# Performance work log

Hardware: AMD Instinct MI355X
Metric: run time of the kernel (lower is better)

Reference implementation:

```python
import jax, jax.numpy as jnp
import numpy as np

B, C, H, W = 8, 256, 128, 128
HEADS, DIM_HEAD = 4, 32
HID = HEADS * DIM_HEAD  # 128


def setup_inputs() -> dict:
    key = jax.random.key(0)
    k1, k2, k3, k4 = jax.random.split(key, 4)
    x = jax.random.normal(k1, (B, C, H, W), dtype=jnp.float32)
    # 1x1 conv weights stored as [out_ch, in_ch]
    w_qkv = jax.random.normal(k2, (3 * HID, C), dtype=jnp.float32) * (1.0 / np.sqrt(C))
    w_out = jax.random.normal(k3, (C, HID), dtype=jnp.float32) * (1.0 / np.sqrt(HID))
    b_out = jax.random.normal(k4, (C,), dtype=jnp.float32) * 0.01
    return {"x": x, "w_qkv": w_qkv, "w_out": w_out, "b_out": b_out}


def reference(x, w_qkv, w_out, b_out):
    b, c, h, w = x.shape
    n = h * w
    # 1x1 conv == channel matmul
    qkv = jnp.einsum('oc,bchw->bohw', w_qkv, x)  # [b, 3*HID, h, w]
    q, k, v = jnp.split(qkv, 3, axis=1)
    # rearrange 'b (heads d) h w -> b heads d (h w)'
    def to_heads(t):
        return t.reshape(b, HEADS, DIM_HEAD, n)
    q, k, v = to_heads(q), to_heads(k), to_heads(v)
    k = jax.nn.softmax(k, axis=-1)  # over spatial n
    # q_scale is False: q used as-is
    context = jnp.einsum('bhdn,bhen->bhde', k, v)   # [b, heads, d, e] small
    out = jnp.einsum('bhde,bhdn->bhen', context, q)  # [b, heads, e, n]
    out = out.reshape(b, HID, h, w)
    out = jnp.einsum('oc,bchw->bohw', w_out, out) + b_out[None, :, None, None]
    return out
```

## Files before the change

kernel.cpp:

```cpp
#include <hip/hip_runtime.h>
#include <stdint.h>

#define BB 8
#define CIN 256
#define NSP 16384
#define HID 128

typedef __bf16 bfrag __attribute__((ext_vector_type(8)));
typedef float  f32x4 __attribute__((ext_vector_type(4)));

__device__ __forceinline__ unsigned short f2bf(float f) {
  union { float f; unsigned int u; } v; v.f = f;
  unsigned int u = v.u;
  return (unsigned short)((u + 0x7FFFu + ((u >> 16) & 1u)) >> 16);
}

__global__ __launch_bounds__(256) void la_prep(const float* __restrict__ w_qkv,
                                               unsigned short* __restrict__ wkvb,
                                               float* __restrict__ zbase) {
  const int blk = blockIdx.x;
  const int t = threadIdx.x;
  if (blk < 64) {
    const int off = (blk * 256 + t) * 4;
    const float4 wv4 = *(const float4*)(w_qkv + (size_t)128 * CIN + off);
    ushort4 p;
    p.x = f2bf(wv4.x); p.y = f2bf(wv4.y); p.z = f2bf(wv4.z); p.w = f2bf(wv4.w);
    *(ushort4*)(wkvb + off) = p;
  } else {
    for (int i = t; i < 8448; i += 256) {
      float4 z = {0.f, 0.f, 0.f, 0.f};
      *(float4*)(zbase + i * 4) = z;
    }
  }
}

__global__ __launch_bounds__(512, 4) void la_fused(const float* __restrict__ x,
                                                   const unsigned short* __restrict__ wkvb,
                                                   float* __restrict__ ctxu,
                                                   float* __restrict__ sums) {
  __shared__ __align__(16) union {
    struct { unsigned short Xb[2][128][40]; } g;
    struct { unsigned short Lk[64][136]; unsigned short Lv[64][136];
             float Pc[4][1024]; } e;
  } sh;
  const int chunk = blockIdx.x;
  const int n0 = chunk * 128;
  const int b = blockIdx.y;
  const int t = threadIdx.x;
  const int lane = t & 63, wv = t >> 6;
  const int l15 = lane & 15, q = lane >> 4;
  const int cl = t & 31;
  const int n16 = (t >> 5) * 8;
  const float* xp = x + (size_t)b * CIN * NSP + n0;
  f32x4 acc[2][8];
#pragma unroll
  for (int i = 0; i < 2; ++i)
#pragma unroll
    for (int j = 0; j < 8; ++j) acc[i][j] = 0.0f;

  float4 xa0, xa1;
  {
    const float* xr = xp + (size_t)cl * NSP + n16;
    xa0 = *(const float4*)xr;
    xa1 = *(const float4*)(xr + 4);
  }
  {
    sh.g.Xb[0][n16 + 0][cl] = f2bf(xa0.x);
    sh.g.Xb[0][n16 + 1][cl] = f2bf(xa0.y);
    sh.g.Xb[0][n16 + 2][cl] = f2bf(xa0.z);
    sh.g.Xb[0][n16 + 3][cl] = f2bf(xa0.w);
    sh.g.Xb[0][n16 + 4][cl] = f2bf(xa1.x);
    sh.g.Xb[0][n16 + 5][cl] = f2bf(xa1.y);
    sh.g.Xb[0][n16 + 6][cl] = f2bf(xa1.z);
    sh.g.Xb[0][n16 + 7][cl] = f2bf(xa1.w);
    const float* xr = xp + (size_t)(32 + cl) * NSP + n16;
    xa0 = *(const float4*)xr;
    xa1 = *(const float4*)(xr + 4);
  }
  __syncthreads();

#pragma unroll
  for (int kc = 0; kc < 8; ++kc) {
    const int p = kc & 1;
    bfrag a0 = *(const bfrag*)(wkvb + (size_t)(wv * 16 + l15) * CIN + kc * 32 + q * 8);
    bfrag a1 = *(const bfrag*)(wkvb + (size_t)(128 + wv * 16 + l15) * CIN + kc * 32 + q * 8);
    if (kc < 7) {
      sh.g.Xb[p ^ 1][n16 + 0][cl] = f2bf(xa0.x);
      sh.g.Xb[p ^ 1][n16 + 1][cl] = f2bf(xa0.y);
      sh.g.Xb[p ^ 1][n16 + 2][cl] = f2bf(xa0.z);
      sh.g.Xb[p ^ 1][n16 + 3][cl] = f2bf(xa0.w);
      sh.g.Xb[p ^ 1][n16 + 4][cl] = f2bf(xa1.x);
      sh.g.Xb[p ^ 1][n16 + 5][cl] = f2bf(xa1.y);
      sh.g.Xb[p ^ 1][n16 + 6][cl] = f2bf(xa1.z);
      sh.g.Xb[p ^ 1][n16 + 7][cl] = f2bf(xa1.w);
      if (kc < 6) {
        const float* xr = xp + (size_t)((kc + 2) * 32 + cl) * NSP + n16;
        xa0 = *(const float4*)xr;
        xa1 = *(const float4*)(xr + 4);
      }
    }
#pragma unroll
    for (int ni = 0; ni < 8; ++ni) {
      bfrag bbv = *(const bfrag*)&sh.g.Xb[p][ni * 16 + l15][q * 8];
      acc[0][ni] = __builtin_amdgcn_mfma_f32_16x16x32_bf16(a0, bbv, acc[0][ni], 0, 0, 0);
      acc[1][ni] = __builtin_amdgcn_mfma_f32_16x16x32_bf16(a1, bbv, acc[1][ni], 0, 0, 0);
    }
    __syncthreads();
  }

#pragma unroll
  for (int ni = 0; ni < 8; ++ni)
#pragma unroll
    for (int rg = 0; rg < 4; ++rg) acc[0][ni][rg] = __expf(acc[0][ni][rg]);

  {
    float sp[4] = {0.f, 0.f, 0.f, 0.f};
#pragma unroll
    for (int ni = 0; ni < 8; ++ni)
#pragma unroll
      for (int rg = 0; rg < 4; ++rg) sp[rg] += acc[0][ni][rg];
#pragma unroll
    for (int rg = 0; rg < 4; ++rg) {
      float s = sp[rg];
      s += __shfl_down(s, 8, 16);
      s += __shfl_down(s, 4, 16);
      s += __shfl_down(s, 2, 16);
      s += __shfl_down(s, 1, 16);
      if (l15 == 0) atomicAdd(&sums[b * 128 + wv * 16 + q * 4 + rg], s);
    }
  }
#pragma unroll
  for (int ph = 0; ph < 2; ++ph) {
    if ((wv >> 2) == ph) {
      const int r = (wv & 3) * 16 + q * 4;
#pragma unroll
      for (int ni = 0; ni < 8; ++ni)
#pragma unroll
        for (int rg = 0; rg < 4; ++rg) {
          sh.e.Lk[r + rg][ni * 16 + l15] = f2bf(acc[0][ni][rg]);
          sh.e.Lv[r + rg][ni * 16 + l15] = f2bf(acc[1][ni][rg]);
        }
    }
    __syncthreads();
    const int hl = wv >> 2, nq = wv & 3;
    f32x4 c2[2][2];
    c2[0][0] = 0.f; c2[0][1] = 0.f; c2[1][0] = 0.f; c2[1][1] = 0.f;
    bfrag ka[2], vb[2];
#pragma unroll
    for (int d2 = 0; d2 < 2; ++d2)
      ka[d2] = *(const bfrag*)&sh.e.Lk[hl * 32 + d2 * 16 + l15][nq * 32 + q * 8];
#pragma unroll
    for (int e2 = 0; e2 < 2; ++e2)
      vb[e2] = *(const bfrag*)&sh.e.Lv[hl * 32 + e2 * 16 + l15][nq * 32 + q * 8];
#pragma unroll
    for (int d2 = 0; d2 < 2; ++d2)
#pragma unroll
      for (int e2 = 0; e2 < 2; ++e2)
        c2[d2][e2] = __builtin_amdgcn_mfma_f32_16x16x32_bf16(ka[d2], vb[e2], c2[d2][e2], 0, 0, 0);
    const int slot = hl * 2 + (nq & 1);
    if (nq < 2) {
#pragma unroll
      for (int d2 = 0; d2 < 2; ++d2)
#pragma unroll
        for (int e2 = 0; e2 < 2; ++e2)
#pragma unroll
          for (int rg = 0; rg < 4; ++rg)
            sh.e.Pc[slot][(d2 * 16 + q * 4 + rg) * 32 + e2 * 16 + l15] = c2[d2][e2][rg];
    }
    __syncthreads();
    if (nq >= 2) {
#pragma unroll
      for (int d2 = 0; d2 < 2; ++d2)
#pragma unroll
        for (int e2 = 0; e2 < 2; ++e2)
#pragma unroll
          for (int rg = 0; rg < 4; ++rg)
            sh.e.Pc[slot][(d2 * 16 + q * 4 + rg) * 32 + e2 * 16 + l15] += c2[d2][e2][rg];
    }
    __syncthreads();
    for (int idx = t; idx < 2048; idx += 512) {
      const int h2 = idx >> 10, pos = idx & 1023;
      atomicAdd(&ctxu[(size_t)b * 4096 + (ph * 2 + h2) * 1024 + pos],
                sh.e.Pc[h2 * 2][pos] + sh.e.Pc[h2 * 2 + 1][pos]);
    }
    __syncthreads();
  }
}

__global__ __launch_bounds__(256) void la_mid(const float* __restrict__ w_out,
                                              const float* __restrict__ ctxu,
                                              const float* __restrict__ sums,
                                              const float* __restrict__ w_qkv,
                                              unsigned short* __restrict__ wcomb) {
  __shared__ float wrow[128];
  const int o = blockIdx.x;
  const int b = blockIdx.y;
  const int t = threadIdx.x;
  if (t < 128) {
    const int h = t >> 5, d = t & 31;
    const float* wr = w_out + (size_t)o * HID + h * 32;
    const float* cr = ctxu + ((size_t)(b * 4 + h) * 32 + d) * 32;
    float s = 0.f;
#pragma unroll 8
    for (int e = 0; e < 32; ++e) s += wr[e] * cr[e];
    wrow[t] = s * (1.0f / sums[b * 128 + t]);
  }
  __syncthreads();
  float s = 0.f;
#pragma unroll 8
  for (int hd = 0; hd < 128; ++hd) s += wrow[hd] * w_qkv[(size_t)hd * CIN + t];
  wcomb[((size_t)b * 256 + o) * 256 + t] = f2bf(s);
}

__global__ __launch_bounds__(512, 4) void la_out(const unsigned short* __restrict__ wcomb,
                                                 const float* __restrict__ x,
                                                 const float* __restrict__ b_out,
                                                 float* __restrict__ out) {
  __shared__ __align__(16) unsigned short Bt[2][128][40];
  const int n0 = blockIdx.x * 128;
  const int b = blockIdx.y;
  const int t = threadIdx.x;
  const int lane = t & 63, wv = t >> 6;
  const int l15 = lane & 15, q = lane >> 4;
  const int wm = (wv & 3) * 64;
  const int wn = (wv >> 2) * 64;
  const int cl = t & 31, n16 = (t >> 5) * 8;
  const float* xp = x + (size_t)b * CIN * NSP + n0;
  const unsigned short* abase = wcomb + (size_t)b * 256 * 256;
  f32x4 acc[4][4];
#pragma unroll
  for (int i = 0; i < 4; ++i)
#pragma unroll
    for (int j = 0; j < 4; ++j) acc[i][j] = 0.0f;

  float4 xa0, xa1;
  {
    const float* xr = xp + (size_t)cl * NSP + n16;
    xa0 = *(const float4*)xr;
    xa1 = *(const float4*)(xr + 4);
  }
  {
    Bt[0][n16 + 0][cl] = f2bf(xa0.x);
    Bt[0][n16 + 1][cl] = f2bf(xa0.y);
    Bt[0][n16 + 2][cl] = f2bf(xa0.z);
    Bt[0][n16 + 3][cl] = f2bf(xa0.w);
    Bt[0][n16 + 4][cl] = f2bf(xa1.x);
    Bt[0][n16 + 5][cl] = f2bf(xa1.y);
    Bt[0][n16 + 6][cl] = f2bf(xa1.z);
    Bt[0][n16 + 7][cl] = f2bf(xa1.w);
    const float* xr = xp + (size_t)(32 + cl) * NSP + n16;
    xa0 = *(const float4*)xr;
    xa1 = *(const float4*)(xr + 4);
  }
  __syncthreads();

#pragma unroll
  for (int kc = 0; kc < 8; ++kc) {
    const int p = kc & 1;
    bfrag a[4];
#pragma unroll
    for (int mi = 0; mi < 4; ++mi)
      a[mi] = *(const bfrag*)(abase + (size_t)(wm + mi * 16 + l15) * 256 + kc * 32 + q * 8);
    if (kc < 7) {
      Bt[p ^ 1][n16 + 0][cl] = f2bf(xa0.x);
      Bt[p ^ 1][n16 + 1][cl] = f2bf(xa0.y);
      Bt[p ^ 1][n16 + 2][cl] = f2bf(xa0.z);
      Bt[p ^ 1][n16 + 3][cl] = f2bf(xa0.w);
      Bt[p ^ 1][n16 + 4][cl] = f2bf(xa1.x);
      Bt[p ^ 1][n16 + 5][cl] = f2bf(xa1.y);
      Bt[p ^ 1][n16 + 6][cl] = f2bf(xa1.z);
      Bt[p ^ 1][n16 + 7][cl] = f2bf(xa1.w);
      if (kc < 6) {
        const float* xr = xp + (size_t)((kc + 2) * 32 + cl) * NSP + n16;
        xa0 = *(const float4*)xr;
        xa1 = *(const float4*)(xr + 4);
      }
    }
#pragma unroll
    for (int ni = 0; ni < 4; ++ni) {
      bfrag bbv = *(const bfrag*)&Bt[p][wn + ni * 16 + l15][q * 8];
#pragma unroll
      for (int mi = 0; mi < 4; ++mi)
        acc[mi][ni] = __builtin_amdgcn_mfma_f32_16x16x32_bf16(a[mi], bbv, acc[mi][ni], 0, 0, 0);
    }
    __syncthreads();
  }
  float* obase = out + (size_t)b * 256 * NSP;
#pragma unroll
  for (int mi = 0; mi < 4; ++mi) {
    const int ob = wm + mi * 16 + q * 4;
    const float4 bias = *(const float4*)(b_out + ob);
    float ba[4] = {bias.x, bias.y, bias.z, bias.w};
#pragma unroll
    for (int ni = 0; ni < 4; ++ni) {
      const int n = n0 + wn + ni * 16 + l15;
#pragma unroll
      for (int rg = 0; rg < 4; ++rg)
        obase[(size_t)(ob + rg) * NSP + n] = acc[mi][ni][rg] + ba[rg];
    }
  }
}


extern "C" void kernel_launch(void* const* d_in, const int* in_sizes, int n_in,
                              void* d_out, int out_size, void* d_ws, size_t ws_size,
                              hipStream_t stream) {
  (void)in_sizes; (void)n_in; (void)out_size; (void)ws_size;
  const float* x     = (const float*)d_in[0];
  const float* w_qkv = (const float*)d_in[1];
  const float* w_out = (const float*)d_in[2];
  const float* b_out = (const float*)d_in[3];
  float* out = (float*)d_out;
  char* ws = (char*)d_ws;
  unsigned short* wkvb  = (unsigned short*)(ws);
  float* ctxu           = (float*)(ws + 131072);
  float* sums           = (float*)(ws + 262144);
  unsigned short* wcomb = (unsigned short*)(ws + 266240);

  la_prep<<<dim3(65), dim3(256), 0, stream>>>(w_qkv, wkvb, ctxu);
  la_fused<<<dim3(NSP / 128, BB), dim3(512), 0, stream>>>(x, wkvb, ctxu, sums);
  la_mid<<<dim3(256, BB), dim3(256), 0, stream>>>(w_out, ctxu, sums, w_qkv, wcomb);
  la_out<<<dim3(NSP / 128, BB), dim3(512), 0, stream>>>(wcomb, x, b_out, out);
}
```

Before: 329.3 us.

## Pre-transpose x to bf16 n-major and stream tiles via global_load_lds

Adds a transpose pass that converts x once into a bf16 [b][n][c] workspace, merged with the weight conversion and zeroing kernel. The fused and output GEMM kernels then read this buffer with direct global-to-LDS 16-byte loads into a four-stage XOR-swizzled ring, replacing per-thread fp32 loads, conversion and scattered 2-byte LDS stores. Each GEMM reads half the bytes, but the extra pass writes 64MB and reads the 128MB x once more, which may cost as much as it saves.

```diff
diff --git a/kernel.cpp b/kernel.cpp
--- a/kernel.cpp
+++ b/kernel.cpp
@@ -8,6 +8,7 @@
 
 typedef __bf16 bfrag __attribute__((ext_vector_type(8)));
 typedef float  f32x4 __attribute__((ext_vector_type(4)));
+typedef unsigned short us8 __attribute__((ext_vector_type(8)));
 
 __device__ __forceinline__ unsigned short f2bf(float f) {
   union { float f; unsigned int u; } v; v.f = f;
@@ -15,13 +16,54 @@
   return (unsigned short)((u + 0x7FFFu + ((u >> 16) & 1u)) >> 16);
 }
 
-__global__ __launch_bounds__(256) void la_prep(const float* __restrict__ w_qkv,
-                                               unsigned short* __restrict__ wkvb,
-                                               float* __restrict__ zbase) {
+__device__ __forceinline__ void gload_lds16(const unsigned short* g, unsigned short* l) {
+  __builtin_amdgcn_global_load_lds((const __attribute__((address_space(1))) void*)g,
+                                   (__attribute__((address_space(3))) void*)l, 16, 0, 0);
+}
+
+#define FENCE() asm volatile("" ::: "memory")
+
+__global__ __launch_bounds__(256) void la_xT(const float* __restrict__ x,
+                                             unsigned short* __restrict__ xT,
+                                             const float* __restrict__ w_qkv,
+                                             unsigned short* __restrict__ wkvb,
+                                             float* __restrict__ zbase) {
+  __shared__ float Xs[64][65];
   const int blk = blockIdx.x;
   const int t = threadIdx.x;
-  if (blk < 64) {
-    const int off = (blk * 256 + t) * 4;
+  if (blk < 8192) {
+    const int b = blk >> 10;
+    const int tile = blk & 1023;
+    const int c0 = (tile & 3) * 64;
+    const int n0 = (tile >> 2) * 64;
+    const float* xb = x + (size_t)b * CIN * NSP;
+    {
+      const int c = t >> 2, nf = (t & 3) * 16;
+      const float* xr = xb + (size_t)(c0 + c) * NSP + n0 + nf;
+#pragma unroll
+      for (int i = 0; i < 4; ++i) {
+        const float4 v = *(const float4*)(xr + i * 4);
+        Xs[c][nf + i * 4 + 0] = v.x;
+        Xs[c][nf + i * 4 + 1] = v.y;
+        Xs[c][nf + i * 4 + 2] = v.z;
+        Xs[c][nf + i * 4 + 3] = v.w;
+      }
+    }
+    __syncthreads();
+    {
+      const int n = t >> 2, c16 = (t & 3) * 16;
+      us8 v0, v1;
+#pragma unroll
+      for (int j = 0; j < 8; ++j) {
+        v0[j] = f2bf(Xs[c16 + j][n]);
+        v1[j] = f2bf(Xs[c16 + 8 + j][n]);
+      }
+      unsigned short* orow = xT + ((size_t)b * NSP + n0 + n) * CIN + c0 + c16;
+      *(us8*)orow = v0;
+      *(us8*)(orow + 8) = v1;
+    }
+  } else if (blk < 8256) {
+    const int off = ((blk - 8192) * 256 + t) * 4;
     const float4 wv4 = *(const float4*)(w_qkv + (size_t)128 * CIN + off);
     ushort4 p;
     p.x = f2bf(wv4.x); p.y = f2bf(wv4.y); p.z = f2bf(wv4.z); p.w = f2bf(wv4.w);
@@ -34,12 +76,12 @@
   }
 }
 
-__global__ __launch_bounds__(512, 4) void la_fused(const float* __restrict__ x,
+__global__ __launch_bounds__(512, 4) void la_fused(const unsigned short* __restrict__ xT,
                                                    const unsigned short* __restrict__ wkvb,
                                                    float* __restrict__ ctxu,
                                                    float* __restrict__ sums) {
   __shared__ __align__(16) union {
-    struct { unsigned short Xb[2][128][40]; } g;
+    unsigned short Sx[4][4096];
     struct { unsigned short Lk[64][136]; unsigned short Lv[64][136];
              float Pc[4][1024]; } e;
   } sh;
@@ -49,63 +91,66 @@
   const int t = threadIdx.x;
   const int lane = t & 63, wv = t >> 6;
   const int l15 = lane & 15, q = lane >> 4;
-  const int cl = t & 31;
-  const int n16 = (t >> 5) * 8;
-  const float* xp = x + (size_t)b * CIN * NSP + n0;
+  const int qs = (q ^ ((l15 >> 1) & 3)) * 8;
+  const unsigned short* xTb = xT + ((size_t)b * NSP + n0) * CIN;
+  const int sn = t >> 2, sc8 = t & 3;
+  const int sc8s = sc8 ^ ((sn >> 1) & 3);
+  const unsigned short* sg = xTb + (size_t)sn * CIN + sc8s * 8;
+  unsigned short* sl = &sh.Sx[0][0] + t * 8;
   f32x4 acc[2][8];
 #pragma unroll
   for (int i = 0; i < 2; ++i)
 #pragma unroll
     for (int j = 0; j < 8; ++j) acc[i][j] = 0.0f;
 
-  float4 xa0, xa1;
-  {
-    const float* xr = xp + (size_t)cl * NSP + n16;
-    xa0 = *(const float4*)xr;
-    xa1 = *(const float4*)(xr + 4);
-  }
-  {
-    sh.g.Xb[0][n16 + 0][cl] = f2bf(xa0.x);
-    sh.g.Xb[0][n16 + 1][cl] = f2bf(xa0.y);
-    sh.g.Xb[0][n16 + 2][cl] = f2bf(xa0.z);
-    sh.g.Xb[0][n16 + 3][cl] = f2bf(xa0.w);
-    sh.g.Xb[0][n16 + 4][cl] = f2bf(xa1.x);
-    sh.g.Xb[0][n16 + 5][cl] = f2bf(xa1.y);
-    sh.g.Xb[0][n16 + 6][cl] = f2bf(xa1.z);
-    sh.g.Xb[0][n16 + 7][cl] = f2bf(xa1.w);
-    const float* xr = xp + (size_t)(32 + cl) * NSP + n16;
-    xa0 = *(const float4*)xr;
-    xa1 = *(const float4*)(xr + 4);
-  }
-  __syncthreads();
-
-#pragma unroll
-  for (int kc = 0; kc < 8; ++kc) {
-    const int p = kc & 1;
+  gload_lds16(sg + 0 * 32, sl + 0 * 4096);
+  gload_lds16(sg + 1 * 32, sl + 1 * 4096);
+  asm volatile("s_waitcnt vmcnt(1)" ::: "memory");
+  __builtin_amdgcn_s_barrier();
+  FENCE();
+
+#pragma unroll
+  for (int kc = 0; kc < 6; ++kc) {
     bfrag a0 = *(const bfrag*)(wkvb + (size_t)(wv * 16 + l15) * CIN + kc * 32 + q * 8);
     bfrag a1 = *(const bfrag*)(wkvb + (size_t)(128 + wv * 16 + l15) * CIN + kc * 32 + q * 8);
-    if (kc < 7) {
-      sh.g.Xb[p ^ 1][n16 + 0][cl] = f2bf(xa0.x);
-      sh.g.Xb[p ^ 1][n16 + 1][cl] = f2bf(xa0.y);
-      sh.g.Xb[p ^ 1][n16 + 2][cl] = f2bf(xa0.z);
-      sh.g.Xb[p ^ 1][n16 + 3][cl] = f2bf(xa0.w);
-      sh.g.Xb[p ^ 1][n16 + 4][cl] = f2bf(xa1.x);
-      sh.g.Xb[p ^ 1][n16 + 5][cl] = f2bf(xa1.y);
-      sh.g.Xb[p ^ 1][n16 + 6][cl] = f2bf(xa1.z);
-      sh.g.Xb[p ^ 1][n16 + 7][cl] = f2bf(xa1.w);
-      if (kc < 6) {
-        const float* xr = xp + (size_t)((kc + 2) * 32 + cl) * NSP + n16;
-        xa0 = *(const float4*)xr;
-        xa1 = *(const float4*)(xr + 4);
-      }
-    }
+    gload_lds16(sg + (kc + 2) * 32, sl + ((kc + 2) & 3) * 4096);
+    const unsigned short* bufp = &sh.Sx[kc & 3][0];
 #pragma unroll
     for (int ni = 0; ni < 8; ++ni) {
-      bfrag bbv = *(const bfrag*)&sh.g.Xb[p][ni * 16 + l15][q * 8];
+      bfrag bbv = *(const bfrag*)(bufp + (ni * 16 + l15) * 32 + qs);
       acc[0][ni] = __builtin_amdgcn_mfma_f32_16x16x32_bf16(a0, bbv, acc[0][ni], 0, 0, 0);
       acc[1][ni] = __builtin_amdgcn_mfma_f32_16x16x32_bf16(a1, bbv, acc[1][ni], 0, 0, 0);
     }
-    __syncthreads();
+    asm volatile("s_waitcnt vmcnt(1)" ::: "memory");
+    __builtin_amdgcn_s_barrier();
+    FENCE();
+  }
+  {
+    bfrag a0 = *(const bfrag*)(wkvb + (size_t)(wv * 16 + l15) * CIN + 6 * 32 + q * 8);
+    bfrag a1 = *(const bfrag*)(wkvb + (size_t)(128 + wv * 16 + l15) * CIN + 6 * 32 + q * 8);
+    const unsigned short* bufp = &sh.Sx[2][0];
+#pragma unroll
+    for (int ni = 0; ni < 8; ++ni) {
+      bfrag bbv = *(const bfrag*)(bufp + (ni * 16 + l15) * 32 + qs);
+      acc[0][ni] = __builtin_amdgcn_mfma_f32_16x16x32_bf16(a0, bbv, acc[0][ni], 0, 0, 0);
+      acc[1][ni] = __builtin_amdgcn_mfma_f32_16x16x32_bf16(a1, bbv, acc[1][ni], 0, 0, 0);
+    }
+    asm volatile("s_waitcnt vmcnt(0)" ::: "memory");
+    __builtin_amdgcn_s_barrier();
+    FENCE();
+  }
+  {
+    bfrag a0 = *(const bfrag*)(wkvb + (size_t)(wv * 16 + l15) * CIN + 7 * 32 + q * 8);
+    bfrag a1 = *(const bfrag*)(wkvb + (size_t)(128 + wv * 16 + l15) * CIN + 7 * 32 + q * 8);
+    const unsigned short* bufp = &sh.Sx[3][0];
+#pragma unroll
+    for (int ni = 0; ni < 8; ++ni) {
+      bfrag bbv = *(const bfrag*)(bufp + (ni * 16 + l15) * 32 + qs);
+      acc[0][ni] = __builtin_amdgcn_mfma_f32_16x16x32_bf16(a0, bbv, acc[0][ni], 0, 0, 0);
+      acc[1][ni] = __builtin_amdgcn_mfma_f32_16x16x32_bf16(a1, bbv, acc[1][ni], 0, 0, 0);
+    }
+    __builtin_amdgcn_s_barrier();
+    FENCE();
   }
 
 #pragma unroll
@@ -213,77 +258,85 @@
 }
 
 __global__ __launch_bounds__(512, 4) void la_out(const unsigned short* __restrict__ wcomb,
-                                                 const float* __restrict__ x,
+                                                 const unsigned short* __restrict__ xT,
                                                  const float* __restrict__ b_out,
                                                  float* __restrict__ out) {
-  __shared__ __align__(16) unsigned short Bt[2][128][40];
+  __shared__ __align__(16) unsigned short Sx[4][4096];
   const int n0 = blockIdx.x * 128;
   const int b = blockIdx.y;
   const int t = threadIdx.x;
   const int lane = t & 63, wv = t >> 6;
   const int l15 = lane & 15, q = lane >> 4;
+  const int qs = (q ^ ((l15 >> 1) & 3)) * 8;
   const int wm = (wv & 3) * 64;
   const int wn = (wv >> 2) * 64;
-  const int cl = t & 31, n16 = (t >> 5) * 8;
-  const float* xp = x + (size_t)b * CIN * NSP + n0;
+  const unsigned short* xTb = xT + ((size_t)b * NSP + n0) * CIN;
   const unsigned short* abase = wcomb + (size_t)b * 256 * 256;
+  const int sn = t >> 2, sc8 = t & 3;
+  const int sc8s = sc8 ^ ((sn >> 1) & 3);
+  const unsigned short* sg = xTb + (size_t)sn * CIN + sc8s * 8;
+  unsigned short* sl = &Sx[0][0] + t * 8;
   f32x4 acc[4][4];
 #pragma unroll
   for (int i = 0; i < 4; ++i)
 #pragma unroll
     for (int j = 0; j < 4; ++j) acc[i][j] = 0.0f;
 
-  float4 xa0, xa1;
-  {
-    const float* xr = xp + (size_t)cl * NSP + n16;
-    xa0 = *(const float4*)xr;
-    xa1 = *(const float4*)(xr + 4);
-  }
-  {
-    Bt[0][n16 + 0][cl] = f2bf(xa0.x);
-    Bt[0][n16 + 1][cl] = f2bf(xa0.y);
-    Bt[0][n16 + 2][cl] = f2bf(xa0.z);
-    Bt[0][n16 + 3][cl] = f2bf(xa0.w);
-    Bt[0][n16 + 4][cl] = f2bf(xa1.x);
-    Bt[0][n16 + 5][cl] = f2bf(xa1.y);
-    Bt[0][n16 + 6][cl] = f2bf(xa1.z);
-    Bt[0][n16 + 7][cl] = f2bf(xa1.w);
-    const float* xr = xp + (size_t)(32 + cl) * NSP + n16;
-    xa0 = *(const float4*)xr;
-    xa1 = *(const float4*)(xr + 4);
-  }
-  __syncthreads();
-
-#pragma unroll
-  for (int kc = 0; kc < 8; ++kc) {
-    const int p = kc & 1;
+  gload_lds16(sg + 0 * 32, sl + 0 * 4096);
+  gload_lds16(sg + 1 * 32, sl + 1 * 4096);
+  asm volatile("s_waitcnt vmcnt(1)" ::: "memory");
+  __builtin_amdgcn_s_barrier();
+  FENCE();
+
+#pragma unroll
+  for (int kc = 0; kc < 6; ++kc) {
     bfrag a[4];
 #pragma unroll
     for (int mi = 0; mi < 4; ++mi)
       a[mi] = *(const bfrag*)(abase + (size_t)(wm + mi * 16 + l15) * 256 + kc * 32 + q * 8);
-    if (kc < 7) {
-      Bt[p ^ 1][n16 + 0][cl] = f2bf(xa0.x);
-      Bt[p ^ 1][n16 + 1][cl] = f2bf(xa0.y);
-      Bt[p ^ 1][n16 + 2][cl] = f2bf(xa0.z);
-      Bt[p ^ 1][n16 + 3][cl] = f2bf(xa0.w);
-      Bt[p ^ 1][n16 + 4][cl] = f2bf(xa1.x);
-      Bt[p ^ 1][n16 + 5][cl] = f2bf(xa1.y);
-      Bt[p ^ 1][n16 + 6][cl] = f2bf(xa1.z);
-      Bt[p ^ 1][n16 + 7][cl] = f2bf(xa1.w);
-      if (kc < 6) {
-        const float* xr = xp + (size_t)((kc + 2) * 32 + cl) * NSP + n16;
-        xa0 = *(const float4*)xr;
-        xa1 = *(const float4*)(xr + 4);
-      }
-    }
+    gload_lds16(sg + (kc + 2) * 32, sl + ((kc + 2) & 3) * 4096);
+    const unsigned short* bufp = &Sx[kc & 3][0];
 #pragma unroll
     for (int ni = 0; ni < 4; ++ni) {
-      bfrag bbv = *(const bfrag*)&Bt[p][wn + ni * 16 + l15][q * 8];
+      bfrag bbv = *(const bfrag*)(bufp + (wn + ni * 16 + l15) * 32 + qs);
 #pragma unroll
       for (int mi = 0; mi < 4; ++mi)
         acc[mi][ni] = __builtin_amdgcn_mfma_f32_16x16x32_bf16(a[mi], bbv, acc[mi][ni], 0, 0, 0);
     }
-    __syncthreads();
+    asm volatile("s_waitcnt vmcnt(1)" ::: "memory");
+    __builtin_amdgcn_s_barrier();
+    FENCE();
+  }
+  {
+    bfrag a[4];
+#pragma unroll
+    for (int mi = 0; mi < 4; ++mi)
+      a[mi] = *(const bfrag*)(abase + (size_t)(wm + mi * 16 + l15) * 256 + 6 * 32 + q * 8);
+    const unsigned short* bufp = &Sx[2][0];
+#pragma unroll
+    for (int ni = 0; ni < 4; ++ni) {
+      bfrag bbv = *(const bfrag*)(bufp + (wn + ni * 16 + l15) * 32 + qs);
+#pragma unroll
+      for (int mi = 0; mi < 4; ++mi)
+        acc[mi][ni] = __builtin_amdgcn_mfma_f32_16x16x32_bf16(a[mi], bbv, acc[mi][ni], 0, 0, 0);
+    }
+    asm volatile("s_waitcnt vmcnt(0)" ::: "memory");
+    __builtin_amdgcn_s_barrier();
+    FENCE();
+  }
+  {
+    bfrag a[4];
+#pragma unroll
+    for (int mi = 0; mi < 4; ++mi)
+      a[mi] = *(const bfrag*)(abase + (size_t)(wm + mi * 16 + l15) * 256 + 7 * 32 + q * 8);
+    const unsigned short* bufp = &Sx[3][0];
+#pragma unroll
+    for (int ni = 0; ni < 4; ++ni) {
+      bfrag bbv = *(const bfrag*)(bufp + (wn + ni * 16 + l15) * 32 + qs);
+#pragma unroll
+      for (int mi = 0; mi < 4; ++mi)
+        acc[mi][ni] = __builtin_amdgcn_mfma_f32_16x16x32_bf16(a[mi], bbv, acc[mi][ni], 0, 0, 0);
+    }
   }
   float* obase = out + (size_t)b * 256 * NSP;
 #pragma unroll
@@ -312,13 +365,14 @@
   const float* b_out = (const float*)d_in[3];
   float* out = (float*)d_out;
   char* ws = (char*)d_ws;
-  unsigned short* wkvb  = (unsigned short*)(ws);
-  float* ctxu           = (float*)(ws + 131072);
-  float* sums           = (float*)(ws + 262144);
-  unsigned short* wcomb = (unsigned short*)(ws + 266240);
-
-  la_prep<<<dim3(65), dim3(256), 0, stream>>>(w_qkv, wkvb, ctxu);
-  la_fused<<<dim3(NSP / 128, BB), dim3(512), 0, stream>>>(x, wkvb, ctxu, sums);
+  unsigned short* xTws  = (unsigned short*)(ws);
+  unsigned short* wkvb  = (unsigned short*)(ws + 67108864);
+  float* ctxu           = (float*)(ws + 67239936);
+  float* sums           = (float*)(ws + 67371008);
+  unsigned short* wcomb = (unsigned short*)(ws + 67375104);
+
+  la_xT<<<dim3(8257), dim3(256), 0, stream>>>(x, xTws, w_qkv, wkvb, ctxu);
+  la_fused<<<dim3(NSP / 128, BB), dim3(512), 0, stream>>>(xTws, wkvb, ctxu, sums);
   la_mid<<<dim3(256, BB), dim3(256), 0, stream>>>(w_out, ctxu, sums, w_qkv, wcomb);
-  la_out<<<dim3(NSP / 128, BB), dim3(512), 0, stream>>>(wcomb, x, b_out, out);
-}
+  la_out<<<dim3(NSP / 128, BB), dim3(512), 0, stream>>>(wcomb, xTws, b_out, out);
+}
```

Measured after the change: 353.2 us. 7.3% more time.

## Halve spatial tile to 64 and simplify context reduction in fused kernel

Applied to the files above, without the earlier changes.

Both the fused K/V projection kernel and the output GEMM kernel now process 64 spatial positions per block instead of 128, which doubles the grid and raises the launch-bounds occupancy hint from 4 to 6 blocks per CU. In the fused kernel, each wave now computes a 16x16 context tile directly from shared K/V and atomically adds it to global memory. This drops the two-phase shared-memory partial-sum staging and its extra barriers. The cost is twice as many global atomics on the context buffer and twice as many reloads of weight fragments per unit of spatial work.

```diff
diff --git a/kernel.cpp b/kernel.cpp
--- a/kernel.cpp
+++ b/kernel.cpp
@@ -34,156 +34,101 @@
   }
 }
 
-__global__ __launch_bounds__(512, 4) void la_fused(const float* __restrict__ x,
+__global__ __launch_bounds__(512, 6) void la_fused(const float* __restrict__ x,
                                                    const unsigned short* __restrict__ wkvb,
                                                    float* __restrict__ ctxu,
                                                    float* __restrict__ sums) {
   __shared__ __align__(16) union {
-    struct { unsigned short Xb[2][128][40]; } g;
-    struct { unsigned short Lk[64][136]; unsigned short Lv[64][136];
-             float Pc[4][1024]; } e;
+    unsigned short Xb[2][64][40];
+    struct { unsigned short Lk[128][72]; unsigned short Lv[128][72]; } e;
   } sh;
   const int chunk = blockIdx.x;
-  const int n0 = chunk * 128;
+  const int n0 = chunk * 64;
   const int b = blockIdx.y;
   const int t = threadIdx.x;
   const int lane = t & 63, wv = t >> 6;
   const int l15 = lane & 15, q = lane >> 4;
-  const int cl = t & 31;
-  const int n16 = (t >> 5) * 8;
+  const int scl = t >> 4;
+  const int snf = (t & 15) * 4;
   const float* xp = x + (size_t)b * CIN * NSP + n0;
-  f32x4 acc[2][8];
+  f32x4 acc[2][4];
 #pragma unroll
   for (int i = 0; i < 2; ++i)
 #pragma unroll
-    for (int j = 0; j < 8; ++j) acc[i][j] = 0.0f;
-
-  float4 xa0, xa1;
+    for (int j = 0; j < 4; ++j) acc[i][j] = 0.0f;
+
+#define STOREX(B, A) do {                         \
+    sh.Xb[B][snf + 0][scl] = f2bf((A).x);         \
+    sh.Xb[B][snf + 1][scl] = f2bf((A).y);         \
+    sh.Xb[B][snf + 2][scl] = f2bf((A).z);         \
+    sh.Xb[B][snf + 3][scl] = f2bf((A).w);         \
+  } while (0)
+
+  float4 xa;
+  xa = *(const float4*)(xp + (size_t)scl * NSP + snf);
+  STOREX(0, xa);
+  xa = *(const float4*)(xp + (size_t)(32 + scl) * NSP + snf);
+  __syncthreads();
+
+#pragma unroll
+  for (int kc = 0; kc < 8; ++kc) {
+    const int buf = kc & 1;
+    if (kc < 7) {
+      STOREX(buf ^ 1, xa);
+      if (kc < 6) xa = *(const float4*)(xp + (size_t)((kc + 2) * 32 + scl) * NSP + snf);
+    }
+    const bfrag a0 = *(const bfrag*)(wkvb + (size_t)(wv * 16 + l15) * CIN + kc * 32 + q * 8);
+    const bfrag a1 = *(const bfrag*)(wkvb + (size_t)(128 + wv * 16 + l15) * CIN + kc * 32 + q * 8);
+#pragma unroll
+    for (int nf = 0; nf < 4; ++nf) {
+      const bfrag bb = *(const bfrag*)&sh.Xb[buf][nf * 16 + l15][q * 8];
+      acc[0][nf] = __builtin_amdgcn_mfma_f32_16x16x32_bf16(a0, bb, acc[0][nf], 0, 0, 0);
+      acc[1][nf] = __builtin_amdgcn_mfma_f32_16x16x32_bf16(a1, bb, acc[1][nf], 0, 0, 0);
+    }
+    __syncthreads();
+  }
+#undef STOREX
+
+#pragma unroll
+  for (int nf = 0; nf < 4; ++nf)
+#pragma unroll
+    for (int rg = 0; rg < 4; ++rg) acc[0][nf][rg] = __expf(acc[0][nf][rg]);
+
+#pragma unroll
+  for (int rg = 0; rg < 4; ++rg) {
+    float s = acc[0][0][rg] + acc[0][1][rg] + acc[0][2][rg] + acc[0][3][rg];
+    s += __shfl_down(s, 8, 16);
+    s += __shfl_down(s, 4, 16);
+    s += __shfl_down(s, 2, 16);
+    s += __shfl_down(s, 1, 16);
+    if (l15 == 0) atomicAdd(&sums[b * 128 + wv * 16 + q * 4 + rg], s);
+  }
+
+#pragma unroll
+  for (int nf = 0; nf < 4; ++nf)
+#pragma unroll
+    for (int rg = 0; rg < 4; ++rg) {
+      sh.e.Lk[wv * 16 + q * 4 + rg][nf * 16 + l15] = f2bf(acc[0][nf][rg]);
+      sh.e.Lv[wv * 16 + q * 4 + rg][nf * 16 + l15] = f2bf(acc[1][nf][rg]);
+    }
+  __syncthreads();
+
   {
-    const float* xr = xp + (size_t)cl * NSP + n16;
-    xa0 = *(const float4*)xr;
-    xa1 = *(const float4*)(xr + 4);
-  }
-  {
-    sh.g.Xb[0][n16 + 0][cl] = f2bf(xa0.x);
-    sh.g.Xb[0][n16 + 1][cl] = f2bf(xa0.y);
-    sh.g.Xb[0][n16 + 2][cl] = f2bf(xa0.z);
-    sh.g.Xb[0][n16 + 3][cl] = f2bf(xa0.w);
-    sh.g.Xb[0][n16 + 4][cl] = f2bf(xa1.x);
-    sh.g.Xb[0][n16 + 5][cl] = f2bf(xa1.y);
-    sh.g.Xb[0][n16 + 6][cl] = f2bf(xa1.z);
-    sh.g.Xb[0][n16 + 7][cl] = f2bf(xa1.w);
-    const float* xr = xp + (size_t)(32 + cl) * NSP + n16;
-    xa0 = *(const float4*)xr;
-    xa1 = *(const float4*)(xr + 4);
-  }
-  __syncthreads();
-
-#pragma unroll
-  for (int kc = 0; kc < 8; ++kc) {
-    const int p = kc & 1;
-    bfrag a0 = *(const bfrag*)(wkvb + (size_t)(wv * 16 + l15) * CIN + kc * 32 + q * 8);
-    bfrag a1 = *(const bfrag*)(wkvb + (size_t)(128 + wv * 16 + l15) * CIN + kc * 32 + q * 8);
-    if (kc < 7) {
-      sh.g.Xb[p ^ 1][n16 + 0][cl] = f2bf(xa0.x);
-      sh.g.Xb[p ^ 1][n16 + 1][cl] = f2bf(xa0.y);
-      sh.g.Xb[p ^ 1][n16 + 2][cl] = f2bf(xa0.z);
-      sh.g.Xb[p ^ 1][n16 + 3][cl] = f2bf(xa0.w);
-      sh.g.Xb[p ^ 1][n16 + 4][cl] = f2bf(xa1.x);
-      sh.g.Xb[p ^ 1][n16 + 5][cl] = f2bf(xa1.y);
-      sh.g.Xb[p ^ 1][n16 + 6][cl] = f2bf(xa1.z);
-      sh.g.Xb[p ^ 1][n16 + 7][cl] = f2bf(xa1.w);
-      if (kc < 6) {
-        const float* xr = xp + (size_t)((kc + 2) * 32 + cl) * NSP + n16;
-        xa0 = *(const float4*)xr;
-        xa1 = *(const float4*)(xr + 4);
-      }
-    }
-#pragma unroll
-    for (int ni = 0; ni < 8; ++ni) {
-      bfrag bbv = *(const bfrag*)&sh.g.Xb[p][ni * 16 + l15][q * 8];
-      acc[0][ni] = __builtin_amdgcn_mfma_f32_16x16x32_bf16(a0, bbv, acc[0][ni], 0, 0, 0);
-      acc[1][ni] = __builtin_amdgcn_mfma_f32_16x16x32_bf16(a1, bbv, acc[1][ni], 0, 0, 0);
-    }
-    __syncthreads();
-  }
-
-#pragma unroll
-  for (int ni = 0; ni < 8; ++ni)
-#pragma unroll
-    for (int rg = 0; rg < 4; ++rg) acc[0][ni][rg] = __expf(acc[0][ni][rg]);
-
-  {
-    float sp[4] = {0.f, 0.f, 0.f, 0.f};
-#pragma unroll
-    for (int ni = 0; ni < 8; ++ni)
-#pragma unroll
-      for (int rg = 0; rg < 4; ++rg) sp[rg] += acc[0][ni][rg];
-#pragma unroll
-    for (int rg = 0; rg < 4; ++rg) {
-      float s = sp[rg];
-      s += __shfl_down(s, 8, 16);
-      s += __shfl_down(s, 4, 16);
-      s += __shfl_down(s, 2, 16);
-      s += __shfl_down(s, 1, 16);
-      if (l15 == 0) atomicAdd(&sums[b * 128 + wv * 16 + q * 4 + rg], s);
-    }
-  }
-#pragma unroll
-  for (int ph = 0; ph < 2; ++ph) {
-    if ((wv >> 2) == ph) {
-      const int r = (wv & 3) * 16 + q * 4;
-#pragma unroll
-      for (int ni = 0; ni < 8; ++ni)
-#pragma unroll
-        for (int rg = 0; rg < 4; ++rg) {
-          sh.e.Lk[r + rg][ni * 16 + l15] = f2bf(acc[0][ni][rg]);
-          sh.e.Lv[r + rg][ni * 16 + l15] = f2bf(acc[1][ni][rg]);
-        }
-    }
-    __syncthreads();
-    const int hl = wv >> 2, nq = wv & 3;
-    f32x4 c2[2][2];
-    c2[0][0] = 0.f; c2[0][1] = 0.f; c2[1][0] = 0.f; c2[1][1] = 0.f;
-    bfrag ka[2], vb[2];
-#pragma unroll
-    for (int d2 = 0; d2 < 2; ++d2)
-      ka[d2] = *(const bfrag*)&sh.e.Lk[hl * 32 + d2 * 16 + l15][nq * 32 + q * 8];
-#pragma unroll
-    for (int e2 = 0; e2 < 2; ++e2)
-      vb[e2] = *(const bfrag*)&sh.e.Lv[hl * 32 + e2 * 16 + l15][nq * 32 + q * 8];
-#pragma unroll
-    for (int d2 = 0; d2 < 2; ++d2)
-#pragma unroll
-      for (int e2 = 0; e2 < 2; ++e2)
-        c2[d2][e2] = __builtin_amdgcn_mfma_f32_16x16x32_bf16(ka[d2], vb[e2], c2[d2][e2], 0, 0, 0);
-    const int slot = hl * 2 + (nq & 1);
-    if (nq < 2) {
-#pragma unroll
-      for (int d2 = 0; d2 < 2; ++d2)
-#pragma unroll
-        for (int e2 = 0; e2 < 2; ++e2)
-#pragma unroll
-          for (int rg = 0; rg < 4; ++rg)
-            sh.e.Pc[slot][(d2 * 16 + q * 4 + rg) * 32 + e2 * 16 + l15] = c2[d2][e2][rg];
-    }
-    __syncthreads();
-    if (nq >= 2) {
-#pragma unroll
-      for (int d2 = 0; d2 < 2; ++d2)
-#pragma unroll
-        for (int e2 = 0; e2 < 2; ++e2)
-#pragma unroll
-          for (int rg = 0; rg < 4; ++rg)
-            sh.e.Pc[slot][(d2 * 16 + q * 4 + rg) * 32 + e2 * 16 + l15] += c2[d2][e2][rg];
-    }
-    __syncthreads();
-    for (int idx = t; idx < 2048; idx += 512) {
-      const int h2 = idx >> 10, pos = idx & 1023;
-      atomicAdd(&ctxu[(size_t)b * 4096 + (ph * 2 + h2) * 1024 + pos],
-                sh.e.Pc[h2 * 2][pos] + sh.e.Pc[h2 * 2 + 1][pos]);
-    }
-    __syncthreads();
+    const int h = wv >> 1, dt = wv & 1;
+    const bfrag ak0 = *(const bfrag*)&sh.e.Lk[h * 32 + dt * 16 + l15][q * 8];
+    const bfrag ak1 = *(const bfrag*)&sh.e.Lk[h * 32 + dt * 16 + l15][32 + q * 8];
+    float* cub = ctxu + (size_t)b * 4096 + h * 1024;
+#pragma unroll
+    for (int et = 0; et < 2; ++et) {
+      const bfrag bv0 = *(const bfrag*)&sh.e.Lv[h * 32 + et * 16 + l15][q * 8];
+      const bfrag bv1 = *(const bfrag*)&sh.e.Lv[h * 32 + et * 16 + l15][32 + q * 8];
+      f32x4 ct = {0.f, 0.f, 0.f, 0.f};
+      ct = __builtin_amdgcn_mfma_f32_16x16x32_bf16(ak0, bv0, ct, 0, 0, 0);
+      ct = __builtin_amdgcn_mfma_f32_16x16x32_bf16(ak1, bv1, ct, 0, 0, 0);
+#pragma unroll
+      for (int rg = 0; rg < 4; ++rg)
+        atomicAdd(&cub[(dt * 16 + q * 4 + rg) * 32 + et * 16 + l15], ct[rg]);
+    }
   }
 }
 
@@ -212,79 +157,62 @@
   wcomb[((size_t)b * 256 + o) * 256 + t] = f2bf(s);
 }
 
-__global__ __launch_bounds__(512, 4) void la_out(const unsigned short* __restrict__ wcomb,
+__global__ __launch_bounds__(512, 6) void la_out(const unsigned short* __restrict__ wcomb,
                                                  const float* __restrict__ x,
                                                  const float* __restrict__ b_out,
                                                  float* __restrict__ out) {
-  __shared__ __align__(16) unsigned short Bt[2][128][40];
-  const int n0 = blockIdx.x * 128;
+  __shared__ __align__(16) unsigned short Bt[2][64][40];
+  const int n0 = blockIdx.x * 64;
   const int b = blockIdx.y;
   const int t = threadIdx.x;
   const int lane = t & 63, wv = t >> 6;
   const int l15 = lane & 15, q = lane >> 4;
   const int wm = (wv & 3) * 64;
-  const int wn = (wv >> 2) * 64;
-  const int cl = t & 31, n16 = (t >> 5) * 8;
+  const int wn = (wv >> 2) * 32;
+  const int scl = t >> 4, snf = (t & 15) * 4;
   const float* xp = x + (size_t)b * CIN * NSP + n0;
   const unsigned short* abase = wcomb + (size_t)b * 256 * 256;
-  f32x4 acc[4][4];
+  f32x4 acc[4][2];
 #pragma unroll
   for (int i = 0; i < 4; ++i)
 #pragma unroll
-    for (int j = 0; j < 4; ++j) acc[i][j] = 0.0f;
-
-  float4 xa0, xa1;
-  {
-    const float* xr = xp + (size_t)cl * NSP + n16;
-    xa0 = *(const float4*)xr;
-    xa1 = *(const float4*)(xr + 4);
-  }
-  {
-    Bt[0][n16 + 0][cl] = f2bf(xa0.x);
-    Bt[0][n16 + 1][cl] = f2bf(xa0.y);
-    Bt[0][n16 + 2][cl] = f2bf(xa0.z);
-    Bt[0][n16 + 3][cl] = f2bf(xa0.w);
-    Bt[0][n16 + 4][cl] = f2bf(xa1.x);
-    Bt[0][n16 + 5][cl] = f2bf(xa1.y);
-    Bt[0][n16 + 6][cl] = f2bf(xa1.z);
-    Bt[0][n16 + 7][cl] = f2bf(xa1.w);
-    const float* xr = xp + (size_t)(32 + cl) * NSP + n16;
-    xa0 = *(const float4*)xr;
-    xa1 = *(const float4*)(xr + 4);
-  }
+    for (int j = 0; j < 2; ++j) acc[i][j] = 0.0f;
+
+#define STOREB(B, A) do {                     \
+    Bt[B][snf + 0][scl] = f2bf((A).x);        \
+    Bt[B][snf + 1][scl] = f2bf((A).y);        \
+    Bt[B][snf + 2][scl] = f2bf((A).z);        \
+    Bt[B][snf + 3][scl] = f2bf((A).w);        \
+  } while (0)
+
+  float4 xa;
+  xa = *(const float4*)(xp + (size_t)scl * NSP + snf);
+  STOREB(0, xa);
+  xa = *(const float4*)(xp + (size_t)(32 + scl) * NSP + snf);
   __syncthreads();
 
 #pragma unroll
   for (int kc = 0; kc < 8; ++kc) {
-    const int p = kc & 1;
+    const int buf = kc & 1;
+    if (kc < 7) {
+      STOREB(buf ^ 1, xa);
+      if (kc < 6) xa = *(const float4*)(xp + (size_t)((kc + 2) * 32 + scl) * NSP + snf);
+    }
     bfrag a[4];
 #pragma unroll
     for (int mi = 0; mi < 4; ++mi)
       a[mi] = *(const bfrag*)(abase + (size_t)(wm + mi * 16 + l15) * 256 + kc * 32 + q * 8);
-    if (kc < 7) {
-      Bt[p ^ 1][n16 + 0][cl] = f2bf(xa0.x);
-      Bt[p ^ 1][n16 + 1][cl] = f2bf(xa0.y);
-      Bt[p ^ 1][n16 + 2][cl] = f2bf(xa0.z);
-      Bt[p ^ 1][n16 + 3][cl] = f2bf(xa0.w);
-      Bt[p ^ 1][n16 + 4][cl] = f2bf(xa1.x);
-      Bt[p ^ 1][n16 + 5][cl] = f2bf(xa1.y);
-      Bt[p ^ 1][n16 + 6][cl] = f2bf(xa1.z);
-      Bt[p ^ 1][n16 + 7][cl] = f2bf(xa1.w);
-      if (kc < 6) {
-        const float* xr = xp + (size_t)((kc + 2) * 32 + cl) * NSP + n16;
-        xa0 = *(const float4*)xr;
-        xa1 = *(const float4*)(xr + 4);
-      }
-    }
-#pragma unroll
-    for (int ni = 0; ni < 4; ++ni) {
-      bfrag bbv = *(const bfrag*)&Bt[p][wn + ni * 16 + l15][q * 8];
+#pragma unroll
+    for (int ni = 0; ni < 2; ++ni) {
+      const bfrag bb = *(const bfrag*)&Bt[buf][wn + ni * 16 + l15][q * 8];
 #pragma unroll
       for (int mi = 0; mi < 4; ++mi)
-        acc[mi][ni] = __builtin_amdgcn_mfma_f32_16x16x32_bf16(a[mi], bbv, acc[mi][ni], 0, 0, 0);
+        acc[mi][ni] = __builtin_amdgcn_mfma_f32_16x16x32_bf16(a[mi], bb, acc[mi][ni], 0, 0, 0);
     }
     __syncthreads();
   }
+#undef STOREB
+
   float* obase = out + (size_t)b * 256 * NSP;
 #pragma unroll
   for (int mi = 0; mi < 4; ++mi) {
@@ -292,7 +220,7 @@
     const float4 bias = *(const float4*)(b_out + ob);
     float ba[4] = {bias.x, bias.y, bias.z, bias.w};
 #pragma unroll
-    for (int ni = 0; ni < 4; ++ni) {
+    for (int ni = 0; ni < 2; ++ni) {
       const int n = n0 + wn + ni * 16 + l15;
 #pragma unroll
       for (int rg = 0; rg < 4; ++rg)
@@ -318,7 +246,7 @@
   unsigned short* wcomb = (unsigned short*)(ws + 266240);
 
   la_prep<<<dim3(65), dim3(256), 0, stream>>>(w_qkv, wkvb, ctxu);
-  la_fused<<<dim3(NSP / 128, BB), dim3(512), 0, stream>>>(x, wkvb, ctxu, sums);
+  la_fused<<<dim3(NSP / 64, BB), dim3(512), 0, stream>>>(x, wkvb, ctxu, sums);
   la_mid<<<dim3(256, BB), dim3(256), 0, stream>>>(w_out, ctxu, sums, w_qkv, wcomb);
-  la_out<<<dim3(NSP / 128, BB), dim3(512), 0, stream>>>(wcomb, x, b_out, out);
-}
+  la_out<<<dim3(NSP / 64, BB), dim3(512), 0, stream>>>(wcomb, x, b_out, out);
+}
```

After: 390.7 us. 18.7% more time.

## Replace global atomic context accumulation with per-chunk partials and a reduce kernel

Applied to the files above, without the earlier changes.

The fused kernel now writes per-chunk partial context matrices and softmax sums to workspace instead of doing global float atomicAdds. A new la_reduce kernel sums the 128 partials per batch, which also removes the zero-init work from la_prep. The LDS row padding for Lk/Lv is also changed from 136 to 140 to alter the bank pattern. This trades atomic contention for about 16 MB of extra partial writes and reads plus one more kernel launch.

```diff
diff --git a/kernel.cpp b/kernel.cpp
--- a/kernel.cpp
+++ b/kernel.cpp
@@ -16,31 +16,23 @@
 }
 
 __global__ __launch_bounds__(256) void la_prep(const float* __restrict__ w_qkv,
-                                               unsigned short* __restrict__ wkvb,
-                                               float* __restrict__ zbase) {
+                                               unsigned short* __restrict__ wkvb) {
   const int blk = blockIdx.x;
   const int t = threadIdx.x;
-  if (blk < 64) {
-    const int off = (blk * 256 + t) * 4;
-    const float4 wv4 = *(const float4*)(w_qkv + (size_t)128 * CIN + off);
-    ushort4 p;
-    p.x = f2bf(wv4.x); p.y = f2bf(wv4.y); p.z = f2bf(wv4.z); p.w = f2bf(wv4.w);
-    *(ushort4*)(wkvb + off) = p;
-  } else {
-    for (int i = t; i < 8448; i += 256) {
-      float4 z = {0.f, 0.f, 0.f, 0.f};
-      *(float4*)(zbase + i * 4) = z;
-    }
-  }
+  const int off = (blk * 256 + t) * 4;
+  const float4 wv4 = *(const float4*)(w_qkv + (size_t)128 * CIN + off);
+  ushort4 p;
+  p.x = f2bf(wv4.x); p.y = f2bf(wv4.y); p.z = f2bf(wv4.z); p.w = f2bf(wv4.w);
+  *(ushort4*)(wkvb + off) = p;
 }
 
 __global__ __launch_bounds__(512, 4) void la_fused(const float* __restrict__ x,
                                                    const unsigned short* __restrict__ wkvb,
-                                                   float* __restrict__ ctxu,
-                                                   float* __restrict__ sums) {
+                                                   float* __restrict__ ctxp,
+                                                   float* __restrict__ sumsp) {
   __shared__ __align__(16) union {
     struct { unsigned short Xb[2][128][40]; } g;
-    struct { unsigned short Lk[64][136]; unsigned short Lv[64][136];
+    struct { unsigned short Lk[64][140]; unsigned short Lv[64][140];
              float Pc[4][1024]; } e;
   } sh;
   const int chunk = blockIdx.x;
@@ -126,9 +118,11 @@
       s += __shfl_down(s, 4, 16);
       s += __shfl_down(s, 2, 16);
       s += __shfl_down(s, 1, 16);
-      if (l15 == 0) atomicAdd(&sums[b * 128 + wv * 16 + q * 4 + rg], s);
-    }
-  }
+      if (l15 == 0)
+        sumsp[((size_t)b * 128 + chunk) * 128 + wv * 16 + q * 4 + rg] = s;
+    }
+  }
+  float* cp = ctxp + ((size_t)b * 128 + chunk) * 4096;
 #pragma unroll
   for (int ph = 0; ph < 2; ++ph) {
     if ((wv >> 2) == ph) {
@@ -180,10 +174,34 @@
     __syncthreads();
     for (int idx = t; idx < 2048; idx += 512) {
       const int h2 = idx >> 10, pos = idx & 1023;
-      atomicAdd(&ctxu[(size_t)b * 4096 + (ph * 2 + h2) * 1024 + pos],
-                sh.e.Pc[h2 * 2][pos] + sh.e.Pc[h2 * 2 + 1][pos]);
-    }
-    __syncthreads();
+      cp[(ph * 2 + h2) * 1024 + pos] = sh.e.Pc[h2 * 2][pos] + sh.e.Pc[h2 * 2 + 1][pos];
+    }
+    __syncthreads();
+  }
+}
+
+__global__ __launch_bounds__(256) void la_reduce(const float* __restrict__ ctxp,
+                                                 const float* __restrict__ sumsp,
+                                                 float* __restrict__ ctxu,
+                                                 float* __restrict__ sums) {
+  const int blk = blockIdx.x;
+  const int t = threadIdx.x;
+  if (blk < 128) {
+    const int gid = blk * 256 + t;
+    const int b = gid >> 12, pos = gid & 4095;
+    const float* base = ctxp + (size_t)b * 128 * 4096 + pos;
+    float s = 0.f;
+#pragma unroll 8
+    for (int c = 0; c < 128; ++c) s += base[(size_t)c * 4096];
+    ctxu[gid] = s;
+  } else {
+    const int gid = (blk - 128) * 256 + t;
+    const int b = gid >> 7, row = gid & 127;
+    const float* base = sumsp + (size_t)b * 128 * 128 + row;
+    float s = 0.f;
+#pragma unroll 8
+    for (int c = 0; c < 128; ++c) s += base[c * 128];
+    sums[gid] = s;
   }
 }
 
@@ -313,12 +331,15 @@
   float* out = (float*)d_out;
   char* ws = (char*)d_ws;
   unsigned short* wkvb  = (unsigned short*)(ws);
-  float* ctxu           = (float*)(ws + 131072);
-  float* sums           = (float*)(ws + 262144);
-  unsigned short* wcomb = (unsigned short*)(ws + 266240);
-
-  la_prep<<<dim3(65), dim3(256), 0, stream>>>(w_qkv, wkvb, ctxu);
-  la_fused<<<dim3(NSP / 128, BB), dim3(512), 0, stream>>>(x, wkvb, ctxu, sums);
+  float* ctxp           = (float*)(ws + 131072);
+  float* sumsp          = (float*)(ws + 16908288);
+  float* ctxu           = (float*)(ws + 17432576);
+  float* sums           = (float*)(ws + 17563648);
+  unsigned short* wcomb = (unsigned short*)(ws + 17567744);
+
+  la_prep<<<dim3(64), dim3(256), 0, stream>>>(w_qkv, wkvb);
+  la_fused<<<dim3(NSP / 128, BB), dim3(512), 0, stream>>>(x, wkvb, ctxp, sumsp);
+  la_reduce<<<dim3(132), dim3(256), 0, stream>>>(ctxp, sumsp, ctxu, sums);
   la_mid<<<dim3(256, BB), dim3(256), 0, stream>>>(w_out, ctxu, sums, w_qkv, wcomb);
   la_out<<<dim3(NSP / 128, BB), dim3(512), 0, stream>>>(wcomb, x, b_out, out);
 }
```

New measurement: 319.4 us. 1.03x faster.
